# Performance work log

Measured on AMD Instinct MI355X. Metric: run time of the kernel, lower is better.

## Reference

```python
import jax, jax.numpy as jnp
import numpy as np

C = 512  # n_channels

def _maxpool2x2(t):
    # t: [B, C, H, W] -> [B, C, H//2, W//2]
    B, Cc, H, W = t.shape
    return t.reshape(B, Cc, H // 2, 2, W // 2, 2).max(axis=(3, 5))

def setup_inputs() -> dict:
    key = jax.random.key(0)
    ks = jax.random.split(key, 6)
    B, H, W = 16, 64, 64
    x = jax.random.normal(ks[0], (B, C, H, W), dtype=jnp.float32)
    # 1x1 conv weights (spectral-normalized convs, no bias) stored as [out, in]
    wq = jax.random.normal(ks[1], (C // 8, C), dtype=jnp.float32) * 0.05
    wk = jax.random.normal(ks[2], (C // 8, C), dtype=jnp.float32) * 0.05
    wv = jax.random.normal(ks[3], (C // 2, C), dtype=jnp.float32) * 0.05
    wo = jax.random.normal(ks[4], (C, C // 2), dtype=jnp.float32) * 0.05
    gamma = jnp.zeros((1,), dtype=jnp.float32) + 0.5  # nonzero so output depends on attention path
    return {"x": x, "wq": wq, "wk": wk, "wv": wv, "wo": wo, "gamma": gamma}

def reference(x, wq, wk, wv, wo, gamma):
    B, Cc, H, W = x.shape
    n = H * W
    # 1x1 convs are channel-mixing matmuls
    f = jnp.einsum('oc,bchw->bohw', wq, x).reshape(B, Cc // 8, n)            # [B, C/8, n]
    g = _maxpool2x2(jnp.einsum('oc,bchw->bohw', wk, x)).reshape(B, Cc // 8, n // 4)  # [B, C/8, n/4]
    h = _maxpool2x2(jnp.einsum('oc,bchw->bohw', wv, x)).reshape(B, Cc // 2, n // 4)  # [B, C/2, n/4]
    # attention: softmax over pooled kv positions
    beta = jax.nn.softmax(jnp.einsum('bcn,bcm->bnm', f, g), axis=-1)         # [B, n, n/4]
    o = jnp.einsum('bcm,bnm->bcn', h, beta).reshape(B, Cc // 2, H, W)        # [B, C/2, H, W]
    o = jnp.einsum('oc,bchw->bohw', wo, o)                                   # [B, C, H, W]
    return gamma.reshape(()) * o + x
```

## Files before the change

kernel.cpp:

```cpp
#include <hip/hip_runtime.h>
#include <cstdint>
#include <cstddef>

namespace {

constexpr int kB  = 16;
constexpr int kC  = 512;
constexpr int kCQ = 64;
constexpr int kCV = 256;
constexpr int kN  = 4096;
constexpr int kM  = 1024;

typedef _Float16 f16;
typedef _Float16 f16x8 __attribute__((ext_vector_type(8)));
typedef float    f32x4 __attribute__((ext_vector_type(4)));

__global__ __launch_bounds__(256)
void convert_weights_kernel(const float* __restrict__ wq,
                            const float* __restrict__ wk,
                            const float* __restrict__ wv,
                            const float* __restrict__ wo,
                            const float* __restrict__ gamma,
                            f16* __restrict__ wcat,
                            f16* __restrict__ woh)
{
    const int idx = blockIdx.x * 256 + threadIdx.x;
    if (idx < 49152) {
        const int e = idx * 4;
        const int r = e >> 9, c = e & 511;
        const float* src = (r < 64)  ? (wq + ((size_t)r << 9))
                         : (r < 128) ? (wk + ((size_t)(r - 64) << 9))
                                     : (wv + ((size_t)(r - 128) << 9));
        float4 v = *(const float4*)(src + c);
        union { f16 h4[4]; uint2 u; } pk;
        pk.h4[0] = (f16)v.x;
        pk.h4[1] = (f16)v.y;
        pk.h4[2] = (f16)v.z;
        pk.h4[3] = (f16)v.w;
        *(uint2*)(wcat + e) = pk.u;
    } else {
        const int e = (idx - 49152) * 4;
        const float g = gamma[0];
        float4 v = *(const float4*)(wo + e);
        union { f16 h4[4]; uint2 u; } pk;
        pk.h4[0] = (f16)(g * v.x);
        pk.h4[1] = (f16)(g * v.y);
        pk.h4[2] = (f16)(g * v.z);
        pk.h4[3] = (f16)(g * v.w);
        *(uint2*)(woh + e) = pk.u;
    }
}

__global__ __launch_bounds__(256)
void proj_pool_mfma(const float* __restrict__ x,
                    const f16* __restrict__ wcat,
                    f16* __restrict__ fT,
                    f16* __restrict__ gT,
                    f16* __restrict__ h)
{
    const int nt  = blockIdx.x;
    const int mt  = blockIdx.y;
    const int b   = blockIdx.z;
    const int tid = threadIdx.x;
    const int w    = tid >> 6;
    const int lane = tid & 63;
    const int quad = lane >> 4;
    const int lq   = lane & 15;
    const int wr   = w >> 1;
    const int wc   = w & 1;

    __shared__ alignas(16) f16 As[128 * 40];
    __shared__ alignas(16) f16 Bs[128 * 40];

    const f16*   Ab = wcat + (size_t)mt * 128 * kC;
    const float* Xb = x + (size_t)b * kC * kN + nt * 128;

    f32x4 acc[4][4];
#pragma unroll
    for (int i = 0; i < 4; ++i)
#pragma unroll
        for (int j = 0; j < 4; ++j) acc[i][j] = {0.f, 0.f, 0.f, 0.f};

    const int sr = tid >> 1;
    const int sk = (tid & 1) * 16;

    uint4 pa0, pa1;
    float tb[16];
    {
        const f16* ap = Ab + (size_t)sr * kC + sk;
        pa0 = *(const uint4*)ap;
        pa1 = *(const uint4*)(ap + 8);
        const float* xp = Xb + (size_t)sk * kN + sr;
#pragma unroll
        for (int j = 0; j < 16; ++j) tb[j] = xp[j * kN];
    }

    for (int ks = 0; ks < 16; ++ks) {
        __syncthreads();
        *(uint4*)&As[sr * 40 + sk]     = pa0;
        *(uint4*)&As[sr * 40 + sk + 8] = pa1;
        {
            f16 tmp[16];
#pragma unroll
            for (int j = 0; j < 16; ++j) tmp[j] = (f16)tb[j];
            *(uint4*)&Bs[sr * 40 + sk]     = *(uint4*)&tmp[0];
            *(uint4*)&Bs[sr * 40 + sk + 8] = *(uint4*)&tmp[8];
        }
        __syncthreads();
        if (ks < 15) {
            const int k0 = (ks + 1) * 32;
            const f16* ap = Ab + (size_t)sr * kC + k0 + sk;
            pa0 = *(const uint4*)ap;
            pa1 = *(const uint4*)(ap + 8);
            const float* xp = Xb + (size_t)(k0 + sk) * kN + sr;
#pragma unroll
            for (int j = 0; j < 16; ++j) tb[j] = xp[j * kN];
        }

        f16x8 af[4], bs[4];
#pragma unroll
        for (int ti = 0; ti < 4; ++ti)
            af[ti] = *(const f16x8*)&As[(wr * 64 + ti * 16 + lq) * 40 + quad * 8];
#pragma unroll
        for (int tj = 0; tj < 4; ++tj) {
            const int col = (tj < 2) ? (wc * 32 + tj * 16 + lq)
                                     : (64 + wc * 32 + (tj - 2) * 16 + lq);
            bs[tj] = *(const f16x8*)&Bs[col * 40 + quad * 8];
        }
        __builtin_amdgcn_s_setprio(1);
#pragma unroll
        for (int ti = 0; ti < 4; ++ti)
#pragma unroll
            for (int tj = 0; tj < 4; ++tj)
                acc[ti][tj] = __builtin_amdgcn_mfma_f32_16x16x32_f16(
                    af[ti], bs[tj], acc[ti][tj], 0, 0, 0);
        __builtin_amdgcn_s_setprio(0);
    }

    if (mt == 0 && wr == 0) {
        f16* fb = fT + (size_t)b * kN * kCQ;
#pragma unroll
        for (int tj = 0; tj < 4; ++tj) {
            const int col = (tj < 2) ? (wc * 32 + tj * 16 + lq)
                                     : (64 + wc * 32 + (tj - 2) * 16 + lq);
            const int n = nt * 128 + col;
#pragma unroll
            for (int ti = 0; ti < 4; ++ti) {
                union { f16 h4[4]; uint2 u; } pk;
#pragma unroll
                for (int r = 0; r < 4; ++r) pk.h4[r] = (f16)acc[ti][tj][r];
                *(uint2*)(fb + (size_t)n * kCQ + ti * 16 + quad * 4) = pk.u;
            }
        }
    } else {
#pragma unroll
        for (int ti = 0; ti < 4; ++ti) {
#pragma unroll
            for (int tjp = 0; tjp < 2; ++tjp) {
                float p[4];
#pragma unroll
                for (int r = 0; r < 4; ++r) {
                    float v = fmaxf(acc[ti][tjp][r], acc[ti][tjp + 2][r]);
                    v = fmaxf(v, __shfl_xor(v, 1, 64));
                    p[r] = v;
                }
                const int m = nt * 32 + wc * 16 + tjp * 8 + (lq >> 1);
                if ((lq & 1) == 0) {
                    if (mt == 0) {
                        union { f16 h4[4]; uint2 u; } pk;
#pragma unroll
                        for (int r = 0; r < 4; ++r) pk.h4[r] = (f16)p[r];
                        *(uint2*)(gT + ((size_t)b * kM + m) * kCQ + ti * 16 + quad * 4) = pk.u;
                    } else {
#pragma unroll
                        for (int r = 0; r < 4; ++r) {
                            const int ch = (mt - 1) * 128 + wr * 64 + ti * 16 + quad * 4 + r;
                            h[((size_t)b * kCV + ch) * kM + m] = (f16)p[r];
                        }
                    }
                }
            }
        }
    }
}

__global__ __launch_bounds__(256, 3)
void attn_out_kernel(const f16* __restrict__ fT,
                     const f16* __restrict__ gT,
                     const f16* __restrict__ hmat,
                     const f16* __restrict__ woh,
                     const float* __restrict__ x,
                     float* __restrict__ out)
{
    const int qt   = blockIdx.x;
    const int b    = blockIdx.y;
    const int tid  = threadIdx.x;
    const int w    = tid >> 6;
    const int lane = tid & 63;
    const int quad = lane >> 4;
    const int lq   = lane & 15;

    __shared__ union alignas(16) SMem {
        struct {
            f16   fsT[64 * 72];
            f16   gsT[32 * 64];
            f16   hs[256 * 40];
            f16   ps[64 * 40];
        } p1;
        struct {
            f16 osT[4 * 16 * 264];
            f16 wos[256 * 40];
        } p2;
    } sm;

    {
        const f16* fb = fT + ((size_t)b * kN + qt * 64) * kCQ;
#pragma unroll
        for (int p = 0; p < 2; ++p) {
            const int unit = tid + p * 256;
            const int q = unit >> 3, u = unit & 7;
            *(uint4*)&sm.p1.fsT[q * 72 + u * 8] = *(const uint4*)(fb + q * 64 + u * 8);
        }
    }
    __syncthreads();

    const f16x8 af0 = *(const f16x8*)&sm.p1.fsT[(w * 16 + lq) * 72 + quad * 8];
    const f16x8 af1 = *(const f16x8*)&sm.p1.fsT[(w * 16 + lq) * 72 + 32 + quad * 8];

    float m_run = -3.0e38f, l_run = 0.f;
    f32x4 o_acc[16];
#pragma unroll
    for (int ci = 0; ci < 16; ++ci) o_acc[ci] = {0.f, 0.f, 0.f, 0.f};

    const f16* gTb = gT + (size_t)b * kM * kCQ;
    const f16* hb  = hmat + (size_t)b * kCV * kM;

    const int gm = tid >> 3, gsu = tid & 7, ggu = gsu ^ (gm & 7);
    const int hc = tid >> 2, hu = tid & 3;
    uint4 pg, ph[4];
    {
        pg = *(const uint4*)(gTb + (size_t)gm * kCQ + ggu * 8);
#pragma unroll
        for (int p = 0; p < 4; ++p)
            ph[p] = *(const uint4*)(hb + (size_t)(hc + p * 64) * kM + hu * 8);
    }

    for (int mi = 0; mi < 32; ++mi) {
        __syncthreads();
        *(uint4*)&sm.p1.gsT[gm * 64 + gsu * 8] = pg;
#pragma unroll
        for (int p = 0; p < 4; ++p)
            *(uint4*)&sm.p1.hs[(hc + p * 64) * 40 + hu * 8] = ph[p];
        __syncthreads();
        if (mi < 31) {
            const int m1 = (mi + 1) * 32;
            pg = *(const uint4*)(gTb + (size_t)(m1 + gm) * kCQ + ggu * 8);
#pragma unroll
            for (int p = 0; p < 4; ++p)
                ph[p] = *(const uint4*)(hb + (size_t)(hc + p * 64) * kM + m1 + hu * 8);
        }

        const int mr0 = lq, mr1 = 16 + lq;
        const f16x8 bg00 = *(const f16x8*)&sm.p1.gsT[mr0 * 64 + ((quad)     ^ (mr0 & 7)) * 8];
        const f16x8 bg01 = *(const f16x8*)&sm.p1.gsT[mr0 * 64 + ((4 + quad) ^ (mr0 & 7)) * 8];
        const f16x8 bg10 = *(const f16x8*)&sm.p1.gsT[mr1 * 64 + ((quad)     ^ (mr1 & 7)) * 8];
        const f16x8 bg11 = *(const f16x8*)&sm.p1.gsT[mr1 * 64 + ((4 + quad) ^ (mr1 & 7)) * 8];
        f32x4 s0 = {0.f, 0.f, 0.f, 0.f}, s1 = {0.f, 0.f, 0.f, 0.f};
        s0 = __builtin_amdgcn_mfma_f32_16x16x32_f16(bg00, af0, s0, 0, 0, 0);
        s0 = __builtin_amdgcn_mfma_f32_16x16x32_f16(bg01, af1, s0, 0, 0, 0);
        s1 = __builtin_amdgcn_mfma_f32_16x16x32_f16(bg10, af0, s1, 0, 0, 0);
        s1 = __builtin_amdgcn_mfma_f32_16x16x32_f16(bg11, af1, s1, 0, 0, 0);

        float cm = fmaxf(fmaxf(fmaxf(s0[0], s0[1]), fmaxf(s0[2], s0[3])),
                         fmaxf(fmaxf(s1[0], s1[1]), fmaxf(s1[2], s1[3])));
        cm = fmaxf(cm, __shfl_xor(cm, 16, 64));
        cm = fmaxf(cm, __shfl_xor(cm, 32, 64));
        const float nm = fmaxf(m_run, cm);
        const float al = __expf(m_run - nm);
        float e0[4], e1[4];
#pragma unroll
        for (int r = 0; r < 4; ++r) { e0[r] = __expf(s0[r] - nm); e1[r] = __expf(s1[r] - nm); }
        float psum = (e0[0] + e0[1]) + (e0[2] + e0[3]) + (e1[0] + e1[1]) + (e1[2] + e1[3]);
        psum += __shfl_xor(psum, 16, 64);
        psum += __shfl_xor(psum, 32, 64);
        m_run = nm;
        l_run = l_run * al + psum;

        union { f16 h4[4]; uint2 u; } pk0, pk1;
#pragma unroll
        for (int r = 0; r < 4; ++r) { pk0.h4[r] = (f16)e0[r]; pk1.h4[r] = (f16)e1[r]; }
        *(uint2*)&sm.p1.ps[(w * 16 + lq) * 40 + quad * 4]      = pk0.u;
        *(uint2*)&sm.p1.ps[(w * 16 + lq) * 40 + 16 + quad * 4] = pk1.u;
        __builtin_amdgcn_sched_barrier(0);

        const f16x8 bp = *(const f16x8*)&sm.p1.ps[(w * 16 + lq) * 40 + quad * 8];
        __builtin_amdgcn_s_setprio(1);
#pragma unroll
        for (int ci = 0; ci < 16; ++ci) {
            const f16x8 ha = *(const f16x8*)&sm.p1.hs[(ci * 16 + lq) * 40 + quad * 8];
            o_acc[ci] *= al;
            o_acc[ci] = __builtin_amdgcn_mfma_f32_16x16x32_f16(ha, bp, o_acc[ci], 0, 0, 0);
        }
        __builtin_amdgcn_s_setprio(0);
    }

    const float inv = 1.0f / l_run;

    const int woc = tid >> 2, wu = tid & 3;
    uint4 pw[4];
#pragma unroll
    for (int p = 0; p < 4; ++p)
        pw[p] = *(const uint4*)(woh + (size_t)(woc + p * 64) * 256 + wu * 8);

    __syncthreads();
#pragma unroll
    for (int ci = 0; ci < 16; ++ci)
#pragma unroll
        for (int r = 0; r < 4; ++r)
            sm.p2.osT[(w * 16 + lq) * 264 + ci * 16 + quad * 4 + r] =
                (f16)(o_acc[ci][r] * inv);

    for (int half = 0; half < 2; ++half) {
        f32x4 acc2[16];
#pragma unroll
        for (int os = 0; os < 16; ++os) acc2[os] = {0.f, 0.f, 0.f, 0.f};

        for (int ck = 0; ck < 8; ++ck) {
            __syncthreads();
#pragma unroll
            for (int p = 0; p < 4; ++p)
                *(uint4*)&sm.p2.wos[(woc + p * 64) * 40 + wu * 8] = pw[p];
            __syncthreads();
            {
                const int s = half * 8 + ck + 1;
                if (s < 16) {
#pragma unroll
                    for (int p = 0; p < 4; ++p)
                        pw[p] = *(const uint4*)(woh +
                            (size_t)((s >> 3) * 256 + woc + p * 64) * 256 +
                            (s & 7) * 32 + wu * 8);
                }
            }
            const f16x8 bo = *(const f16x8*)&sm.p2.osT[(w * 16 + lq) * 264 + ck * 32 + quad * 8];
            __builtin_amdgcn_s_setprio(1);
#pragma unroll
            for (int os = 0; os < 16; ++os) {
                const f16x8 wa = *(const f16x8*)&sm.p2.wos[(os * 16 + lq) * 40 + quad * 8];
                acc2[os] = __builtin_amdgcn_mfma_f32_16x16x32_f16(wa, bo, acc2[os], 0, 0, 0);
            }
            __builtin_amdgcn_s_setprio(0);
        }

        const int n0 = qt * 64 + w * 16 + lq;
#pragma unroll
        for (int os = 0; os < 16; ++os) {
#pragma unroll
            for (int r = 0; r < 4; ++r) {
                const int oc = half * 256 + os * 16 + quad * 4 + r;
                const size_t idx = ((size_t)b * kC + oc) * (size_t)kN + n0;
                out[idx] = acc2[os][r] + x[idx];
            }
        }
    }
}

}

extern "C" void kernel_launch(void* const* d_in, const int* in_sizes, int n_in,
                              void* d_out, int out_size, void* d_ws, size_t ws_size,
                              hipStream_t stream) {
    const float* x     = (const float*)d_in[0];
    const float* wq    = (const float*)d_in[1];
    const float* wk    = (const float*)d_in[2];
    const float* wv    = (const float*)d_in[3];
    const float* wo    = (const float*)d_in[4];
    const float* gamma = (const float*)d_in[5];
    float* out = (float*)d_out;

    f16* fT   = (f16*)d_ws;
    f16* gT   = fT  + (size_t)kB * kN * kCQ;
    f16* hw   = gT  + (size_t)kB * kM * kCQ;
    f16* woh  = hw  + (size_t)kB * kCV * kM;
    f16* wcat = woh + (size_t)kC * kCV;

    hipLaunchKernelGGL(convert_weights_kernel, dim3(320), dim3(256), 0, stream,
                       wq, wk, wv, wo, gamma, wcat, woh);
    hipLaunchKernelGGL(proj_pool_mfma, dim3(32, 3, kB), dim3(256), 0, stream,
                       x, wcat, fT, gT, hw);
    hipLaunchKernelGGL(attn_out_kernel, dim3(64, kB), dim3(256), 0, stream,
                       fT, gT, hw, woh, x, out);
}
```

Before: 523.9 us.

## Fuse projection M-tiles per block and process two query tiles per attention block

The projection kernel now computes all 384 output channels (f, g and h) in one 512-thread block. Each x tile is read from global memory and converted to fp16 once, instead of once per channel-group block. The attention kernel now handles 128 queries per block as two 64-query sub-tiles, each with its own online-softmax state, sharing every staged g/h tile and the wo tiles. In exchange, accumulator register pressure doubles, the attention grid halves to 512 blocks with occupancy hint 2, and the shared-memory footprint grows.

```diff
diff --git a/kernel.cpp b/kernel.cpp
--- a/kernel.cpp
+++ b/kernel.cpp
@@ -51,7 +51,7 @@
     }
 }
 
-__global__ __launch_bounds__(256)
+__global__ __launch_bounds__(512, 2)
 void proj_pool_mfma(const float* __restrict__ x,
                     const f16* __restrict__ wcat,
                     f16* __restrict__ fT,
@@ -59,8 +59,7 @@
                     f16* __restrict__ h)
 {
     const int nt  = blockIdx.x;
-    const int mt  = blockIdx.y;
-    const int b   = blockIdx.z;
+    const int b   = blockIdx.y;
     const int tid = threadIdx.x;
     const int w    = tid >> 6;
     const int lane = tid & 63;
@@ -69,92 +68,94 @@
     const int wr   = w >> 1;
     const int wc   = w & 1;
 
-    __shared__ alignas(16) f16 As[128 * 40];
+    __shared__ alignas(16) f16 As[384 * 40];
     __shared__ alignas(16) f16 Bs[128 * 40];
 
-    const f16*   Ab = wcat + (size_t)mt * 128 * kC;
     const float* Xb = x + (size_t)b * kC * kN + nt * 128;
 
-    f32x4 acc[4][4];
-#pragma unroll
-    for (int i = 0; i < 4; ++i)
+    f32x4 acc[6][4];
+#pragma unroll
+    for (int i = 0; i < 6; ++i)
 #pragma unroll
         for (int j = 0; j < 4; ++j) acc[i][j] = {0.f, 0.f, 0.f, 0.f};
 
-    const int sr = tid >> 1;
-    const int sk = (tid & 1) * 16;
-
-    uint4 pa0, pa1;
-    float tb[16];
-    {
-        const f16* ap = Ab + (size_t)sr * kC + sk;
-        pa0 = *(const uint4*)ap;
-        pa1 = *(const uint4*)(ap + 8);
-        const float* xp = Xb + (size_t)sk * kN + sr;
-#pragma unroll
-        for (int j = 0; j < 16; ++j) tb[j] = xp[j * kN];
-    }
+    const int bn = tid & 127;
+    const int kg = tid >> 7;
+
+    uint4 pa[3];
+    float xv[8];
+#pragma unroll
+    for (int p = 0; p < 3; ++p) {
+        const int unit = tid + p * 512;
+        const int row = unit >> 2, su = unit & 3;
+        pa[p] = *(const uint4*)(wcat + (size_t)row * kC + su * 8);
+    }
+#pragma unroll
+    for (int j = 0; j < 8; ++j) xv[j] = Xb[(size_t)(kg * 8 + j) * kN + bn];
 
     for (int ks = 0; ks < 16; ++ks) {
         __syncthreads();
-        *(uint4*)&As[sr * 40 + sk]     = pa0;
-        *(uint4*)&As[sr * 40 + sk + 8] = pa1;
+#pragma unroll
+        for (int p = 0; p < 3; ++p) {
+            const int unit = tid + p * 512;
+            const int row = unit >> 2, su = unit & 3;
+            *(uint4*)&As[row * 40 + su * 8] = pa[p];
+        }
         {
-            f16 tmp[16];
-#pragma unroll
-            for (int j = 0; j < 16; ++j) tmp[j] = (f16)tb[j];
-            *(uint4*)&Bs[sr * 40 + sk]     = *(uint4*)&tmp[0];
-            *(uint4*)&Bs[sr * 40 + sk + 8] = *(uint4*)&tmp[8];
+            union { f16 hh[8]; uint4 u; } pk;
+#pragma unroll
+            for (int j = 0; j < 8; ++j) pk.hh[j] = (f16)xv[j];
+            *(uint4*)&Bs[bn * 40 + kg * 8] = pk.u;
         }
         __syncthreads();
         if (ks < 15) {
             const int k0 = (ks + 1) * 32;
-            const f16* ap = Ab + (size_t)sr * kC + k0 + sk;
-            pa0 = *(const uint4*)ap;
-            pa1 = *(const uint4*)(ap + 8);
-            const float* xp = Xb + (size_t)(k0 + sk) * kN + sr;
-#pragma unroll
-            for (int j = 0; j < 16; ++j) tb[j] = xp[j * kN];
-        }
-
-        f16x8 af[4], bs[4];
-#pragma unroll
-        for (int ti = 0; ti < 4; ++ti)
-            af[ti] = *(const f16x8*)&As[(wr * 64 + ti * 16 + lq) * 40 + quad * 8];
+#pragma unroll
+            for (int p = 0; p < 3; ++p) {
+                const int unit = tid + p * 512;
+                const int row = unit >> 2, su = unit & 3;
+                pa[p] = *(const uint4*)(wcat + (size_t)row * kC + k0 + su * 8);
+            }
+#pragma unroll
+            for (int j = 0; j < 8; ++j)
+                xv[j] = Xb[(size_t)(k0 + kg * 8 + j) * kN + bn];
+        }
+
+        f16x8 bsv[4];
 #pragma unroll
         for (int tj = 0; tj < 4; ++tj) {
             const int col = (tj < 2) ? (wc * 32 + tj * 16 + lq)
                                      : (64 + wc * 32 + (tj - 2) * 16 + lq);
-            bs[tj] = *(const f16x8*)&Bs[col * 40 + quad * 8];
+            bsv[tj] = *(const f16x8*)&Bs[col * 40 + quad * 8];
         }
         __builtin_amdgcn_s_setprio(1);
 #pragma unroll
-        for (int ti = 0; ti < 4; ++ti)
+        for (int ti = 0; ti < 6; ++ti) {
+            const f16x8 af = *(const f16x8*)&As[(wr * 96 + ti * 16 + lq) * 40 + quad * 8];
 #pragma unroll
             for (int tj = 0; tj < 4; ++tj)
                 acc[ti][tj] = __builtin_amdgcn_mfma_f32_16x16x32_f16(
-                    af[ti], bs[tj], acc[ti][tj], 0, 0, 0);
+                    af, bsv[tj], acc[ti][tj], 0, 0, 0);
+        }
         __builtin_amdgcn_s_setprio(0);
     }
 
-    if (mt == 0 && wr == 0) {
-        f16* fb = fT + (size_t)b * kN * kCQ;
-#pragma unroll
-        for (int tj = 0; tj < 4; ++tj) {
-            const int col = (tj < 2) ? (wc * 32 + tj * 16 + lq)
-                                     : (64 + wc * 32 + (tj - 2) * 16 + lq);
-            const int n = nt * 128 + col;
-#pragma unroll
-            for (int ti = 0; ti < 4; ++ti) {
+#pragma unroll
+    for (int ti = 0; ti < 6; ++ti) {
+        const int ch0 = wr * 96 + ti * 16;
+        if (ch0 < 64) {
+            f16* fb = fT + (size_t)b * kN * kCQ;
+#pragma unroll
+            for (int tj = 0; tj < 4; ++tj) {
+                const int col = (tj < 2) ? (wc * 32 + tj * 16 + lq)
+                                         : (64 + wc * 32 + (tj - 2) * 16 + lq);
+                const int n = nt * 128 + col;
                 union { f16 h4[4]; uint2 u; } pk;
 #pragma unroll
                 for (int r = 0; r < 4; ++r) pk.h4[r] = (f16)acc[ti][tj][r];
-                *(uint2*)(fb + (size_t)n * kCQ + ti * 16 + quad * 4) = pk.u;
-            }
-        }
-    } else {
-#pragma unroll
-        for (int ti = 0; ti < 4; ++ti) {
+                *(uint2*)(fb + (size_t)n * kCQ + ch0 + quad * 4) = pk.u;
+            }
+        } else {
 #pragma unroll
             for (int tjp = 0; tjp < 2; ++tjp) {
                 float p[4];
@@ -166,15 +167,15 @@
                 }
                 const int m = nt * 32 + wc * 16 + tjp * 8 + (lq >> 1);
                 if ((lq & 1) == 0) {
-                    if (mt == 0) {
+                    if (ch0 < 128) {
                         union { f16 h4[4]; uint2 u; } pk;
 #pragma unroll
                         for (int r = 0; r < 4; ++r) pk.h4[r] = (f16)p[r];
-                        *(uint2*)(gT + ((size_t)b * kM + m) * kCQ + ti * 16 + quad * 4) = pk.u;
+                        *(uint2*)(gT + ((size_t)b * kM + m) * kCQ + (ch0 - 64) + quad * 4) = pk.u;
                     } else {
 #pragma unroll
                         for (int r = 0; r < 4; ++r) {
-                            const int ch = (mt - 1) * 128 + wr * 64 + ti * 16 + quad * 4 + r;
+                            const int ch = ch0 - 128 + quad * 4 + r;
                             h[((size_t)b * kCV + ch) * kM + m] = (f16)p[r];
                         }
                     }
@@ -184,7 +185,7 @@
     }
 }
 
-__global__ __launch_bounds__(256, 3)
+__global__ __launch_bounds__(256, 2)
 void attn_out_kernel(const f16* __restrict__ fT,
                      const f16* __restrict__ gT,
                      const f16* __restrict__ hmat,
@@ -202,21 +203,21 @@
 
     __shared__ union alignas(16) SMem {
         struct {
-            f16   fsT[64 * 72];
+            f16   fsT[128 * 72];
             f16   gsT[32 * 64];
             f16   hs[256 * 40];
             f16   ps[64 * 40];
         } p1;
         struct {
-            f16 osT[4 * 16 * 264];
+            f16 osT[64 * 264];
             f16 wos[256 * 40];
         } p2;
     } sm;
 
     {
-        const f16* fb = fT + ((size_t)b * kN + qt * 64) * kCQ;
-#pragma unroll
-        for (int p = 0; p < 2; ++p) {
+        const f16* fb = fT + ((size_t)b * kN + qt * 128) * kCQ;
+#pragma unroll
+        for (int p = 0; p < 4; ++p) {
             const int unit = tid + p * 256;
             const int q = unit >> 3, u = unit & 7;
             *(uint4*)&sm.p1.fsT[q * 72 + u * 8] = *(const uint4*)(fb + q * 64 + u * 8);
@@ -224,13 +225,18 @@
     }
     __syncthreads();
 
-    const f16x8 af0 = *(const f16x8*)&sm.p1.fsT[(w * 16 + lq) * 72 + quad * 8];
-    const f16x8 af1 = *(const f16x8*)&sm.p1.fsT[(w * 16 + lq) * 72 + 32 + quad * 8];
-
-    float m_run = -3.0e38f, l_run = 0.f;
-    f32x4 o_acc[16];
-#pragma unroll
-    for (int ci = 0; ci < 16; ++ci) o_acc[ci] = {0.f, 0.f, 0.f, 0.f};
+    const f16x8 afA0 = *(const f16x8*)&sm.p1.fsT[(w * 16 + lq) * 72 + quad * 8];
+    const f16x8 afA1 = *(const f16x8*)&sm.p1.fsT[(w * 16 + lq) * 72 + 32 + quad * 8];
+    const f16x8 afB0 = *(const f16x8*)&sm.p1.fsT[(64 + w * 16 + lq) * 72 + quad * 8];
+    const f16x8 afB1 = *(const f16x8*)&sm.p1.fsT[(64 + w * 16 + lq) * 72 + 32 + quad * 8];
+
+    float mA = -3.0e38f, lA = 0.f, mB = -3.0e38f, lB = 0.f;
+    f32x4 o_accA[16], o_accB[16];
+#pragma unroll
+    for (int ci = 0; ci < 16; ++ci) {
+        o_accA[ci] = {0.f, 0.f, 0.f, 0.f};
+        o_accB[ci] = {0.f, 0.f, 0.f, 0.f};
+    }
 
     const f16* gTb = gT + (size_t)b * kM * kCQ;
     const f16* hb  = hmat + (size_t)b * kCV * kM;
@@ -265,46 +271,81 @@
         const f16x8 bg01 = *(const f16x8*)&sm.p1.gsT[mr0 * 64 + ((4 + quad) ^ (mr0 & 7)) * 8];
         const f16x8 bg10 = *(const f16x8*)&sm.p1.gsT[mr1 * 64 + ((quad)     ^ (mr1 & 7)) * 8];
         const f16x8 bg11 = *(const f16x8*)&sm.p1.gsT[mr1 * 64 + ((4 + quad) ^ (mr1 & 7)) * 8];
-        f32x4 s0 = {0.f, 0.f, 0.f, 0.f}, s1 = {0.f, 0.f, 0.f, 0.f};
-        s0 = __builtin_amdgcn_mfma_f32_16x16x32_f16(bg00, af0, s0, 0, 0, 0);
-        s0 = __builtin_amdgcn_mfma_f32_16x16x32_f16(bg01, af1, s0, 0, 0, 0);
-        s1 = __builtin_amdgcn_mfma_f32_16x16x32_f16(bg10, af0, s1, 0, 0, 0);
-        s1 = __builtin_amdgcn_mfma_f32_16x16x32_f16(bg11, af1, s1, 0, 0, 0);
-
-        float cm = fmaxf(fmaxf(fmaxf(s0[0], s0[1]), fmaxf(s0[2], s0[3])),
-                         fmaxf(fmaxf(s1[0], s1[1]), fmaxf(s1[2], s1[3])));
-        cm = fmaxf(cm, __shfl_xor(cm, 16, 64));
-        cm = fmaxf(cm, __shfl_xor(cm, 32, 64));
-        const float nm = fmaxf(m_run, cm);
-        const float al = __expf(m_run - nm);
-        float e0[4], e1[4];
-#pragma unroll
-        for (int r = 0; r < 4; ++r) { e0[r] = __expf(s0[r] - nm); e1[r] = __expf(s1[r] - nm); }
-        float psum = (e0[0] + e0[1]) + (e0[2] + e0[3]) + (e1[0] + e1[1]) + (e1[2] + e1[3]);
-        psum += __shfl_xor(psum, 16, 64);
-        psum += __shfl_xor(psum, 32, 64);
-        m_run = nm;
-        l_run = l_run * al + psum;
-
-        union { f16 h4[4]; uint2 u; } pk0, pk1;
-#pragma unroll
-        for (int r = 0; r < 4; ++r) { pk0.h4[r] = (f16)e0[r]; pk1.h4[r] = (f16)e1[r]; }
-        *(uint2*)&sm.p1.ps[(w * 16 + lq) * 40 + quad * 4]      = pk0.u;
-        *(uint2*)&sm.p1.ps[(w * 16 + lq) * 40 + 16 + quad * 4] = pk1.u;
+        f32x4 s0A = {0.f,0.f,0.f,0.f}, s1A = {0.f,0.f,0.f,0.f};
+        f32x4 s0B = {0.f,0.f,0.f,0.f}, s1B = {0.f,0.f,0.f,0.f};
+        s0A = __builtin_amdgcn_mfma_f32_16x16x32_f16(bg00, afA0, s0A, 0, 0, 0);
+        s0A = __builtin_amdgcn_mfma_f32_16x16x32_f16(bg01, afA1, s0A, 0, 0, 0);
+        s1A = __builtin_amdgcn_mfma_f32_16x16x32_f16(bg10, afA0, s1A, 0, 0, 0);
+        s1A = __builtin_amdgcn_mfma_f32_16x16x32_f16(bg11, afA1, s1A, 0, 0, 0);
+        s0B = __builtin_amdgcn_mfma_f32_16x16x32_f16(bg00, afB0, s0B, 0, 0, 0);
+        s0B = __builtin_amdgcn_mfma_f32_16x16x32_f16(bg01, afB1, s0B, 0, 0, 0);
+        s1B = __builtin_amdgcn_mfma_f32_16x16x32_f16(bg10, afB0, s1B, 0, 0, 0);
+        s1B = __builtin_amdgcn_mfma_f32_16x16x32_f16(bg11, afB1, s1B, 0, 0, 0);
+
+        float alA;
+        {
+            float cm = fmaxf(fmaxf(fmaxf(s0A[0], s0A[1]), fmaxf(s0A[2], s0A[3])),
+                             fmaxf(fmaxf(s1A[0], s1A[1]), fmaxf(s1A[2], s1A[3])));
+            cm = fmaxf(cm, __shfl_xor(cm, 16, 64));
+            cm = fmaxf(cm, __shfl_xor(cm, 32, 64));
+            const float nm = fmaxf(mA, cm);
+            alA = __expf(mA - nm);
+            float e0[4], e1[4];
+#pragma unroll
+            for (int r = 0; r < 4; ++r) { e0[r] = __expf(s0A[r] - nm); e1[r] = __expf(s1A[r] - nm); }
+            float psum = (e0[0]+e0[1])+(e0[2]+e0[3])+(e1[0]+e1[1])+(e1[2]+e1[3]);
+            psum += __shfl_xor(psum, 16, 64);
+            psum += __shfl_xor(psum, 32, 64);
+            mA = nm;
+            lA = lA * alA + psum;
+            union { f16 h4[4]; uint2 u; } pk0, pk1;
+#pragma unroll
+            for (int r = 0; r < 4; ++r) { pk0.h4[r] = (f16)e0[r]; pk1.h4[r] = (f16)e1[r]; }
+            *(uint2*)&sm.p1.ps[(w * 16 + lq) * 40 + quad * 4]      = pk0.u;
+            *(uint2*)&sm.p1.ps[(w * 16 + lq) * 40 + 16 + quad * 4] = pk1.u;
+        }
+        const f16x8 bpA = *(const f16x8*)&sm.p1.ps[(w * 16 + lq) * 40 + quad * 8];
         __builtin_amdgcn_sched_barrier(0);
 
-        const f16x8 bp = *(const f16x8*)&sm.p1.ps[(w * 16 + lq) * 40 + quad * 8];
+        float alB;
+        {
+            float cm = fmaxf(fmaxf(fmaxf(s0B[0], s0B[1]), fmaxf(s0B[2], s0B[3])),
+                             fmaxf(fmaxf(s1B[0], s1B[1]), fmaxf(s1B[2], s1B[3])));
+            cm = fmaxf(cm, __shfl_xor(cm, 16, 64));
+            cm = fmaxf(cm, __shfl_xor(cm, 32, 64));
+            const float nm = fmaxf(mB, cm);
+            alB = __expf(mB - nm);
+            float e0[4], e1[4];
+#pragma unroll
+            for (int r = 0; r < 4; ++r) { e0[r] = __expf(s0B[r] - nm); e1[r] = __expf(s1B[r] - nm); }
+            float psum = (e0[0]+e0[1])+(e0[2]+e0[3])+(e1[0]+e1[1])+(e1[2]+e1[3]);
+            psum += __shfl_xor(psum, 16, 64);
+            psum += __shfl_xor(psum, 32, 64);
+            mB = nm;
+            lB = lB * alB + psum;
+            union { f16 h4[4]; uint2 u; } pk0, pk1;
+#pragma unroll
+            for (int r = 0; r < 4; ++r) { pk0.h4[r] = (f16)e0[r]; pk1.h4[r] = (f16)e1[r]; }
+            *(uint2*)&sm.p1.ps[(w * 16 + lq) * 40 + quad * 4]      = pk0.u;
+            *(uint2*)&sm.p1.ps[(w * 16 + lq) * 40 + 16 + quad * 4] = pk1.u;
+        }
+        const f16x8 bpB = *(const f16x8*)&sm.p1.ps[(w * 16 + lq) * 40 + quad * 8];
+        __builtin_amdgcn_sched_barrier(0);
+
         __builtin_amdgcn_s_setprio(1);
 #pragma unroll
         for (int ci = 0; ci < 16; ++ci) {
             const f16x8 ha = *(const f16x8*)&sm.p1.hs[(ci * 16 + lq) * 40 + quad * 8];
-            o_acc[ci] *= al;
-            o_acc[ci] = __builtin_amdgcn_mfma_f32_16x16x32_f16(ha, bp, o_acc[ci], 0, 0, 0);
+            o_accA[ci] *= alA;
+            o_accA[ci] = __builtin_amdgcn_mfma_f32_16x16x32_f16(ha, bpA, o_accA[ci], 0, 0, 0);
+            o_accB[ci] *= alB;
+            o_accB[ci] = __builtin_amdgcn_mfma_f32_16x16x32_f16(ha, bpB, o_accB[ci], 0, 0, 0);
         }
         __builtin_amdgcn_s_setprio(0);
     }
 
-    const float inv = 1.0f / l_run;
+    const float invA = 1.0f / lA;
+    const float invB = 1.0f / lB;
 
     const int woc = tid >> 2, wu = tid & 3;
     uint4 pw[4];
@@ -313,52 +354,65 @@
         pw[p] = *(const uint4*)(woh + (size_t)(woc + p * 64) * 256 + wu * 8);
 
     __syncthreads();
-#pragma unroll
-    for (int ci = 0; ci < 16; ++ci)
-#pragma unroll
-        for (int r = 0; r < 4; ++r)
-            sm.p2.osT[(w * 16 + lq) * 264 + ci * 16 + quad * 4 + r] =
-                (f16)(o_acc[ci][r] * inv);
-
-    for (int half = 0; half < 2; ++half) {
-        f32x4 acc2[16];
-#pragma unroll
-        for (int os = 0; os < 16; ++os) acc2[os] = {0.f, 0.f, 0.f, 0.f};
-
-        for (int ck = 0; ck < 8; ++ck) {
-            __syncthreads();
-#pragma unroll
-            for (int p = 0; p < 4; ++p)
-                *(uint4*)&sm.p2.wos[(woc + p * 64) * 40 + wu * 8] = pw[p];
-            __syncthreads();
-            {
-                const int s = half * 8 + ck + 1;
-                if (s < 16) {
+
+#pragma unroll
+    for (int ci = 0; ci < 16; ++ci) {
+        union { f16 h4[4]; uint2 u; } pk;
+#pragma unroll
+        for (int r = 0; r < 4; ++r) pk.h4[r] = (f16)(o_accA[ci][r] * invA);
+        *(uint2*)&sm.p2.osT[(w * 16 + lq) * 264 + ci * 16 + quad * 4] = pk.u;
+    }
+
+    int s = 0;
+    for (int tile = 0; tile < 2; ++tile) {
+        for (int half = 0; half < 2; ++half) {
+            f32x4 acc2[16];
+#pragma unroll
+            for (int os = 0; os < 16; ++os) acc2[os] = {0.f, 0.f, 0.f, 0.f};
+
+            for (int ck = 0; ck < 8; ++ck) {
+                __syncthreads();
+#pragma unroll
+                for (int p = 0; p < 4; ++p)
+                    *(uint4*)&sm.p2.wos[(woc + p * 64) * 40 + wu * 8] = pw[p];
+                __syncthreads();
+                ++s;
+                if (s < 32) {
+                    const int sp = s & 15;
 #pragma unroll
                     for (int p = 0; p < 4; ++p)
                         pw[p] = *(const uint4*)(woh +
-                            (size_t)((s >> 3) * 256 + woc + p * 64) * 256 +
-                            (s & 7) * 32 + wu * 8);
+                            (size_t)((sp >> 3) * 256 + woc + p * 64) * 256 +
+                            (sp & 7) * 32 + wu * 8);
                 }
-            }
-            const f16x8 bo = *(const f16x8*)&sm.p2.osT[(w * 16 + lq) * 264 + ck * 32 + quad * 8];
-            __builtin_amdgcn_s_setprio(1);
+                const f16x8 bo = *(const f16x8*)&sm.p2.osT[(w * 16 + lq) * 264 + ck * 32 + quad * 8];
+                __builtin_amdgcn_s_setprio(1);
+#pragma unroll
+                for (int os = 0; os < 16; ++os) {
+                    const f16x8 wa = *(const f16x8*)&sm.p2.wos[(os * 16 + lq) * 40 + quad * 8];
+                    acc2[os] = __builtin_amdgcn_mfma_f32_16x16x32_f16(wa, bo, acc2[os], 0, 0, 0);
+                }
+                __builtin_amdgcn_s_setprio(0);
+            }
+
+            const int n0 = qt * 128 + tile * 64 + w * 16 + lq;
 #pragma unroll
             for (int os = 0; os < 16; ++os) {
-                const f16x8 wa = *(const f16x8*)&sm.p2.wos[(os * 16 + lq) * 40 + quad * 8];
-                acc2[os] = __builtin_amdgcn_mfma_f32_16x16x32_f16(wa, bo, acc2[os], 0, 0, 0);
-            }
-            __builtin_amdgcn_s_setprio(0);
-        }
-
-        const int n0 = qt * 64 + w * 16 + lq;
-#pragma unroll
-        for (int os = 0; os < 16; ++os) {
-#pragma unroll
-            for (int r = 0; r < 4; ++r) {
-                const int oc = half * 256 + os * 16 + quad * 4 + r;
-                const size_t idx = ((size_t)b * kC + oc) * (size_t)kN + n0;
-                out[idx] = acc2[os][r] + x[idx];
+#pragma unroll
+                for (int r = 0; r < 4; ++r) {
+                    const int oc = half * 256 + os * 16 + quad * 4 + r;
+                    const size_t idx = ((size_t)b * kC + oc) * (size_t)kN + n0;
+                    out[idx] = acc2[os][r] + x[idx];
+                }
+            }
+        }
+        if (tile == 0) {
+#pragma unroll
+            for (int ci = 0; ci < 16; ++ci) {
+                union { f16 h4[4]; uint2 u; } pk;
+#pragma unroll
+                for (int r = 0; r < 4; ++r) pk.h4[r] = (f16)(o_accB[ci][r] * invB);
+                *(uint2*)&sm.p2.osT[(w * 16 + lq) * 264 + ci * 16 + quad * 4] = pk.u;
             }
         }
     }
@@ -385,8 +439,8 @@
 
     hipLaunchKernelGGL(convert_weights_kernel, dim3(320), dim3(256), 0, stream,
                        wq, wk, wv, wo, gamma, wcat, woh);
-    hipLaunchKernelGGL(proj_pool_mfma, dim3(32, 3, kB), dim3(256), 0, stream,
+    hipLaunchKernelGGL(proj_pool_mfma, dim3(32, kB), dim3(512), 0, stream,
                        x, wcat, fT, gT, hw);
-    hipLaunchKernelGGL(attn_out_kernel, dim3(64, kB), dim3(256), 0, stream,
+    hipLaunchKernelGGL(attn_out_kernel, dim3(32, kB), dim3(256), 0, stream,
                        fT, gT, hw, woh, x, out);
 }
```

New measurement: 472.3 us. 9.8% less time.

## Double-buffer LDS with direct global-to-LDS loads and retile projection kernel

Applied to the files above, without the earlier changes.

The projection kernel moves to 512-thread blocks, each covering 192 output channels, so the grid shrinks from 3 to 2 channel tiles. Weight tiles are copied straight into a double-buffered, XOR-swizzled LDS through global_load_lds, which leaves one barrier per k-step. The attention kernel does the same for the g/h tiles, loads f directly into registers, and reads the wo weights from global memory instead of staging them in LDS. The aim is fewer barriers and register round-trips and better overlap of loads with MFMA work. The cost is more uncoalesced or L2-dependent global reads for wo, plus correctness risk in the swizzle addressing of the direct-to-LDS writes.

```diff
diff --git a/kernel.cpp b/kernel.cpp
--- a/kernel.cpp
+++ b/kernel.cpp
@@ -14,6 +14,13 @@
 typedef _Float16 f16;
 typedef _Float16 f16x8 __attribute__((ext_vector_type(8)));
 typedef float    f32x4 __attribute__((ext_vector_type(4)));
+
+__device__ __forceinline__ void gload16(const f16* g, f16* l) {
+    __builtin_amdgcn_global_load_lds(
+        (const __attribute__((address_space(1))) void*)g,
+        (__attribute__((address_space(3))) void*)l,
+        16, 0, 0);
+}
 
 __global__ __launch_bounds__(256)
 void convert_weights_kernel(const float* __restrict__ wq,
@@ -33,25 +40,21 @@
                                      : (wv + ((size_t)(r - 128) << 9));
         float4 v = *(const float4*)(src + c);
         union { f16 h4[4]; uint2 u; } pk;
-        pk.h4[0] = (f16)v.x;
-        pk.h4[1] = (f16)v.y;
-        pk.h4[2] = (f16)v.z;
-        pk.h4[3] = (f16)v.w;
+        pk.h4[0] = (f16)v.x; pk.h4[1] = (f16)v.y;
+        pk.h4[2] = (f16)v.z; pk.h4[3] = (f16)v.w;
         *(uint2*)(wcat + e) = pk.u;
     } else {
         const int e = (idx - 49152) * 4;
         const float g = gamma[0];
         float4 v = *(const float4*)(wo + e);
         union { f16 h4[4]; uint2 u; } pk;
-        pk.h4[0] = (f16)(g * v.x);
-        pk.h4[1] = (f16)(g * v.y);
-        pk.h4[2] = (f16)(g * v.z);
-        pk.h4[3] = (f16)(g * v.w);
+        pk.h4[0] = (f16)(g * v.x); pk.h4[1] = (f16)(g * v.y);
+        pk.h4[2] = (f16)(g * v.z); pk.h4[3] = (f16)(g * v.w);
         *(uint2*)(woh + e) = pk.u;
     }
 }
 
-__global__ __launch_bounds__(256)
+__global__ __launch_bounds__(512, 4)
 void proj_pool_mfma(const float* __restrict__ x,
                     const f16* __restrict__ wcat,
                     f16* __restrict__ fT,
@@ -69,92 +72,98 @@
     const int wr   = w >> 1;
     const int wc   = w & 1;
 
-    __shared__ alignas(16) f16 As[128 * 40];
-    __shared__ alignas(16) f16 Bs[128 * 40];
-
-    const f16*   Ab = wcat + (size_t)mt * 128 * kC;
+    __shared__ alignas(16) f16 As[2][192 * 32];
+    __shared__ alignas(16) f16 Bs[2][128 * 36];
+
+    const f16*   Ab = wcat + (size_t)mt * 192 * kC;
     const float* Xb = x + (size_t)b * kC * kN + nt * 128;
 
-    f32x4 acc[4][4];
-#pragma unroll
-    for (int i = 0; i < 4; ++i)
+    f32x4 acc[3][4];
+#pragma unroll
+    for (int i = 0; i < 3; ++i)
 #pragma unroll
         for (int j = 0; j < 4; ++j) acc[i][j] = {0.f, 0.f, 0.f, 0.f};
 
-    const int sr = tid >> 1;
-    const int sk = (tid & 1) * 16;
-
-    uint4 pa0, pa1;
-    float tb[16];
-    {
-        const f16* ap = Ab + (size_t)sr * kC + sk;
-        pa0 = *(const uint4*)ap;
-        pa1 = *(const uint4*)(ap + 8);
-        const float* xp = Xb + (size_t)sk * kN + sr;
-#pragma unroll
-        for (int j = 0; j < 16; ++j) tb[j] = xp[j * kN];
-    }
+    const int bn = tid & 127;
+    const int kg = tid >> 7;
+    float xv[8];
+
+    auto stageA = [&](int buf, int k0) {
+        {
+            const int u = tid;
+            const int row = u >> 2, g = u & 3;
+            gload16(Ab + (size_t)row * kC + k0 + ((g ^ (row & 3)) * 8),
+                    &As[buf][(w * 64) * 8]);
+        }
+        if (tid < 256) {
+            const int u = 512 + tid;
+            const int row = u >> 2, g = u & 3;
+            gload16(Ab + (size_t)row * kC + k0 + ((g ^ (row & 3)) * 8),
+                    &As[buf][(512 + w * 64) * 8]);
+        }
+    };
+    auto loadB = [&](int k0) {
+#pragma unroll
+        for (int j = 0; j < 8; ++j) xv[j] = Xb[(size_t)(k0 + kg * 8 + j) * kN + bn];
+    };
+    auto writeB = [&](int buf) {
+        union { f16 hh[8]; uint4 u; } pk;
+#pragma unroll
+        for (int j = 0; j < 8; ++j) pk.hh[j] = (f16)xv[j];
+        *(uint4*)&Bs[buf][bn * 36 + kg * 8] = pk.u;
+    };
+
+    stageA(0, 0);
+    loadB(0);
+    writeB(0);
+    __syncthreads();
 
     for (int ks = 0; ks < 16; ++ks) {
-        __syncthreads();
-        *(uint4*)&As[sr * 40 + sk]     = pa0;
-        *(uint4*)&As[sr * 40 + sk + 8] = pa1;
-        {
-            f16 tmp[16];
-#pragma unroll
-            for (int j = 0; j < 16; ++j) tmp[j] = (f16)tb[j];
-            *(uint4*)&Bs[sr * 40 + sk]     = *(uint4*)&tmp[0];
-            *(uint4*)&Bs[sr * 40 + sk + 8] = *(uint4*)&tmp[8];
-        }
-        __syncthreads();
+        const int cur = ks & 1;
         if (ks < 15) {
-            const int k0 = (ks + 1) * 32;
-            const f16* ap = Ab + (size_t)sr * kC + k0 + sk;
-            pa0 = *(const uint4*)ap;
-            pa1 = *(const uint4*)(ap + 8);
-            const float* xp = Xb + (size_t)(k0 + sk) * kN + sr;
-#pragma unroll
-            for (int j = 0; j < 16; ++j) tb[j] = xp[j * kN];
-        }
-
-        f16x8 af[4], bs[4];
-#pragma unroll
-        for (int ti = 0; ti < 4; ++ti)
-            af[ti] = *(const f16x8*)&As[(wr * 64 + ti * 16 + lq) * 40 + quad * 8];
+            stageA(cur ^ 1, (ks + 1) * 32);
+            loadB((ks + 1) * 32);
+        }
+
+        f16x8 bsv[4];
 #pragma unroll
         for (int tj = 0; tj < 4; ++tj) {
             const int col = (tj < 2) ? (wc * 32 + tj * 16 + lq)
                                      : (64 + wc * 32 + (tj - 2) * 16 + lq);
-            bs[tj] = *(const f16x8*)&Bs[col * 40 + quad * 8];
+            bsv[tj] = *(const f16x8*)&Bs[cur][col * 36 + quad * 8];
         }
         __builtin_amdgcn_s_setprio(1);
 #pragma unroll
-        for (int ti = 0; ti < 4; ++ti)
+        for (int ti = 0; ti < 3; ++ti) {
+            const int row = wr * 48 + ti * 16 + lq;
+            const f16x8 af = *(const f16x8*)&As[cur][row * 32 + ((quad ^ (row & 3)) * 8)];
 #pragma unroll
             for (int tj = 0; tj < 4; ++tj)
                 acc[ti][tj] = __builtin_amdgcn_mfma_f32_16x16x32_f16(
-                    af[ti], bs[tj], acc[ti][tj], 0, 0, 0);
+                    af, bsv[tj], acc[ti][tj], 0, 0, 0);
+        }
         __builtin_amdgcn_s_setprio(0);
-    }
-
-    if (mt == 0 && wr == 0) {
-        f16* fb = fT + (size_t)b * kN * kCQ;
-#pragma unroll
-        for (int tj = 0; tj < 4; ++tj) {
-            const int col = (tj < 2) ? (wc * 32 + tj * 16 + lq)
-                                     : (64 + wc * 32 + (tj - 2) * 16 + lq);
-            const int n = nt * 128 + col;
-#pragma unroll
-            for (int ti = 0; ti < 4; ++ti) {
+
+        if (ks < 15) writeB(cur ^ 1);
+        __syncthreads();
+    }
+
+#pragma unroll
+    for (int ti = 0; ti < 3; ++ti) {
+        const int ch0 = mt * 192 + wr * 48 + ti * 16;
+        if (ch0 < 64) {
+            f16* fb = fT + (size_t)b * kN * kCQ;
+#pragma unroll
+            for (int tj = 0; tj < 4; ++tj) {
+                const int col = (tj < 2) ? (wc * 32 + tj * 16 + lq)
+                                         : (64 + wc * 32 + (tj - 2) * 16 + lq);
+                const int n = nt * 128 + col;
                 union { f16 h4[4]; uint2 u; } pk;
 #pragma unroll
                 for (int r = 0; r < 4; ++r) pk.h4[r] = (f16)acc[ti][tj][r];
-                *(uint2*)(fb + (size_t)n * kCQ + ti * 16 + quad * 4) = pk.u;
+                *(uint2*)(fb + (size_t)n * kCQ + ch0 + quad * 4) = pk.u;
             }
-        }
-    } else {
-#pragma unroll
-        for (int ti = 0; ti < 4; ++ti) {
+        } else {
 #pragma unroll
             for (int tjp = 0; tjp < 2; ++tjp) {
                 float p[4];
@@ -166,15 +175,15 @@
                 }
                 const int m = nt * 32 + wc * 16 + tjp * 8 + (lq >> 1);
                 if ((lq & 1) == 0) {
-                    if (mt == 0) {
+                    if (ch0 < 128) {
                         union { f16 h4[4]; uint2 u; } pk;
 #pragma unroll
                         for (int r = 0; r < 4; ++r) pk.h4[r] = (f16)p[r];
-                        *(uint2*)(gT + ((size_t)b * kM + m) * kCQ + ti * 16 + quad * 4) = pk.u;
+                        *(uint2*)(gT + ((size_t)b * kM + m) * kCQ + (ch0 - 64) + quad * 4) = pk.u;
                     } else {
 #pragma unroll
                         for (int r = 0; r < 4; ++r) {
-                            const int ch = (mt - 1) * 128 + wr * 64 + ti * 16 + quad * 4 + r;
+                            const int ch = ch0 - 128 + quad * 4 + r;
                             h[((size_t)b * kCV + ch) * kM + m] = (f16)p[r];
                         }
                     }
@@ -202,30 +211,19 @@
 
     __shared__ union alignas(16) SMem {
         struct {
-            f16   fsT[64 * 72];
-            f16   gsT[32 * 64];
-            f16   hs[256 * 40];
-            f16   ps[64 * 40];
+            f16 gs[2][32 * 64];
+            f16 hs[2][256 * 32];
+            f16 ps[64 * 36];
         } p1;
         struct {
-            f16 osT[4 * 16 * 264];
-            f16 wos[256 * 40];
+            f16 osT[64 * 260];
         } p2;
     } sm;
 
-    {
-        const f16* fb = fT + ((size_t)b * kN + qt * 64) * kCQ;
-#pragma unroll
-        for (int p = 0; p < 2; ++p) {
-            const int unit = tid + p * 256;
-            const int q = unit >> 3, u = unit & 7;
-            *(uint4*)&sm.p1.fsT[q * 72 + u * 8] = *(const uint4*)(fb + q * 64 + u * 8);
-        }
-    }
-    __syncthreads();
-
-    const f16x8 af0 = *(const f16x8*)&sm.p1.fsT[(w * 16 + lq) * 72 + quad * 8];
-    const f16x8 af1 = *(const f16x8*)&sm.p1.fsT[(w * 16 + lq) * 72 + 32 + quad * 8];
+    const int q = qt * 64 + w * 16 + lq;
+    const f16* fq = fT + ((size_t)b * kN + q) * kCQ;
+    const f16x8 af0 = *(const f16x8*)(fq + quad * 8);
+    const f16x8 af1 = *(const f16x8*)(fq + 32 + quad * 8);
 
     float m_run = -3.0e38f, l_run = 0.f;
     f32x4 o_acc[16];
@@ -235,36 +233,34 @@
     const f16* gTb = gT + (size_t)b * kM * kCQ;
     const f16* hb  = hmat + (size_t)b * kCV * kM;
 
-    const int gm = tid >> 3, gsu = tid & 7, ggu = gsu ^ (gm & 7);
-    const int hc = tid >> 2, hu = tid & 3;
-    uint4 pg, ph[4];
-    {
-        pg = *(const uint4*)(gTb + (size_t)gm * kCQ + ggu * 8);
-#pragma unroll
-        for (int p = 0; p < 4; ++p)
-            ph[p] = *(const uint4*)(hb + (size_t)(hc + p * 64) * kM + hu * 8);
-    }
+    auto stage = [&](int buf, int m0) {
+        {
+            const int m = tid >> 3, g = tid & 7;
+            gload16(gTb + (size_t)(m0 + m) * kCQ + ((g ^ (m & 7)) * 8),
+                    &sm.p1.gs[buf][(w * 64) * 8]);
+        }
+#pragma unroll
+        for (int p = 0; p < 4; ++p) {
+            const int u = p * 256 + tid;
+            const int c = u >> 2, g = u & 3;
+            gload16(hb + (size_t)c * kM + m0 + ((g ^ (c & 3)) * 8),
+                    &sm.p1.hs[buf][(p * 256 + w * 64) * 8]);
+        }
+    };
+
+    stage(0, 0);
+    __syncthreads();
 
     for (int mi = 0; mi < 32; ++mi) {
-        __syncthreads();
-        *(uint4*)&sm.p1.gsT[gm * 64 + gsu * 8] = pg;
-#pragma unroll
-        for (int p = 0; p < 4; ++p)
-            *(uint4*)&sm.p1.hs[(hc + p * 64) * 40 + hu * 8] = ph[p];
-        __syncthreads();
-        if (mi < 31) {
-            const int m1 = (mi + 1) * 32;
-            pg = *(const uint4*)(gTb + (size_t)(m1 + gm) * kCQ + ggu * 8);
-#pragma unroll
-            for (int p = 0; p < 4; ++p)
-                ph[p] = *(const uint4*)(hb + (size_t)(hc + p * 64) * kM + m1 + hu * 8);
-        }
+        const int cur = mi & 1;
+        if (mi < 31) stage(cur ^ 1, (mi + 1) * 32);
 
         const int mr0 = lq, mr1 = 16 + lq;
-        const f16x8 bg00 = *(const f16x8*)&sm.p1.gsT[mr0 * 64 + ((quad)     ^ (mr0 & 7)) * 8];
-        const f16x8 bg01 = *(const f16x8*)&sm.p1.gsT[mr0 * 64 + ((4 + quad) ^ (mr0 & 7)) * 8];
-        const f16x8 bg10 = *(const f16x8*)&sm.p1.gsT[mr1 * 64 + ((quad)     ^ (mr1 & 7)) * 8];
-        const f16x8 bg11 = *(const f16x8*)&sm.p1.gsT[mr1 * 64 + ((4 + quad) ^ (mr1 & 7)) * 8];
+        const f16* gsc = &sm.p1.gs[cur][0];
+        const f16x8 bg00 = *(const f16x8*)&gsc[mr0 * 64 + ((quad       ^ (mr0 & 7)) * 8)];
+        const f16x8 bg01 = *(const f16x8*)&gsc[mr0 * 64 + (((4 + quad) ^ (mr0 & 7)) * 8)];
+        const f16x8 bg10 = *(const f16x8*)&gsc[mr1 * 64 + ((quad       ^ (mr1 & 7)) * 8)];
+        const f16x8 bg11 = *(const f16x8*)&gsc[mr1 * 64 + (((4 + quad) ^ (mr1 & 7)) * 8)];
         f32x4 s0 = {0.f, 0.f, 0.f, 0.f}, s1 = {0.f, 0.f, 0.f, 0.f};
         s0 = __builtin_amdgcn_mfma_f32_16x16x32_f16(bg00, af0, s0, 0, 0, 0);
         s0 = __builtin_amdgcn_mfma_f32_16x16x32_f16(bg01, af1, s0, 0, 0, 0);
@@ -289,36 +285,32 @@
         union { f16 h4[4]; uint2 u; } pk0, pk1;
 #pragma unroll
         for (int r = 0; r < 4; ++r) { pk0.h4[r] = (f16)e0[r]; pk1.h4[r] = (f16)e1[r]; }
-        *(uint2*)&sm.p1.ps[(w * 16 + lq) * 40 + quad * 4]      = pk0.u;
-        *(uint2*)&sm.p1.ps[(w * 16 + lq) * 40 + 16 + quad * 4] = pk1.u;
+        *(uint2*)&sm.p1.ps[(w * 16 + lq) * 36 + quad * 4]      = pk0.u;
+        *(uint2*)&sm.p1.ps[(w * 16 + lq) * 36 + 16 + quad * 4] = pk1.u;
         __builtin_amdgcn_sched_barrier(0);
-
-        const f16x8 bp = *(const f16x8*)&sm.p1.ps[(w * 16 + lq) * 40 + quad * 8];
+        const f16x8 bp = *(const f16x8*)&sm.p1.ps[(w * 16 + lq) * 36 + quad * 8];
+
         __builtin_amdgcn_s_setprio(1);
 #pragma unroll
         for (int ci = 0; ci < 16; ++ci) {
-            const f16x8 ha = *(const f16x8*)&sm.p1.hs[(ci * 16 + lq) * 40 + quad * 8];
+            const int c = ci * 16 + lq;
+            const f16x8 ha = *(const f16x8*)&sm.p1.hs[cur][c * 32 + ((quad ^ (lq & 3)) * 8)];
             o_acc[ci] *= al;
             o_acc[ci] = __builtin_amdgcn_mfma_f32_16x16x32_f16(ha, bp, o_acc[ci], 0, 0, 0);
         }
         __builtin_amdgcn_s_setprio(0);
+
+        __syncthreads();
     }
 
     const float inv = 1.0f / l_run;
-
-    const int woc = tid >> 2, wu = tid & 3;
-    uint4 pw[4];
-#pragma unroll
-    for (int p = 0; p < 4; ++p)
-        pw[p] = *(const uint4*)(woh + (size_t)(woc + p * 64) * 256 + wu * 8);
-
-    __syncthreads();
-#pragma unroll
-    for (int ci = 0; ci < 16; ++ci)
-#pragma unroll
-        for (int r = 0; r < 4; ++r)
-            sm.p2.osT[(w * 16 + lq) * 264 + ci * 16 + quad * 4 + r] =
-                (f16)(o_acc[ci][r] * inv);
+#pragma unroll
+    for (int ci = 0; ci < 16; ++ci) {
+        union { f16 h4[4]; uint2 u; } pk;
+#pragma unroll
+        for (int r = 0; r < 4; ++r) pk.h4[r] = (f16)(o_acc[ci][r] * inv);
+        *(uint2*)&sm.p2.osT[(w * 16 + lq) * 260 + ci * 16 + quad * 4] = pk.u;
+    }
 
     for (int half = 0; half < 2; ++half) {
         f32x4 acc2[16];
@@ -326,26 +318,12 @@
         for (int os = 0; os < 16; ++os) acc2[os] = {0.f, 0.f, 0.f, 0.f};
 
         for (int ck = 0; ck < 8; ++ck) {
-            __syncthreads();
-#pragma unroll
-            for (int p = 0; p < 4; ++p)
-                *(uint4*)&sm.p2.wos[(woc + p * 64) * 40 + wu * 8] = pw[p];
-            __syncthreads();
-            {
-                const int s = half * 8 + ck + 1;
-                if (s < 16) {
-#pragma unroll
-                    for (int p = 0; p < 4; ++p)
-                        pw[p] = *(const uint4*)(woh +
-                            (size_t)((s >> 3) * 256 + woc + p * 64) * 256 +
-                            (s & 7) * 32 + wu * 8);
-                }
-            }
-            const f16x8 bo = *(const f16x8*)&sm.p2.osT[(w * 16 + lq) * 264 + ck * 32 + quad * 8];
+            const f16x8 bo = *(const f16x8*)&sm.p2.osT[(w * 16 + lq) * 260 + ck * 32 + quad * 8];
             __builtin_amdgcn_s_setprio(1);
 #pragma unroll
             for (int os = 0; os < 16; ++os) {
-                const f16x8 wa = *(const f16x8*)&sm.p2.wos[(os * 16 + lq) * 40 + quad * 8];
+                const f16x8 wa = *(const f16x8*)(woh +
+                    (size_t)(half * 256 + os * 16 + lq) * 256 + ck * 32 + quad * 8);
                 acc2[os] = __builtin_amdgcn_mfma_f32_16x16x32_f16(wa, bo, acc2[os], 0, 0, 0);
             }
             __builtin_amdgcn_s_setprio(0);
@@ -385,7 +363,7 @@
 
     hipLaunchKernelGGL(convert_weights_kernel, dim3(320), dim3(256), 0, stream,
                        wq, wk, wv, wo, gamma, wcat, woh);
-    hipLaunchKernelGGL(proj_pool_mfma, dim3(32, 3, kB), dim3(256), 0, stream,
+    hipLaunchKernelGGL(proj_pool_mfma, dim3(32, 2, kB), dim3(512), 0, stream,
                        x, wcat, fT, gT, hw);
     hipLaunchKernelGGL(attn_out_kernel, dim3(64, kB), dim3(256), 0, stream,
                        fT, gT, hw, woh, x, out);
```

After: 532.9 us. About the same (+1.7%).
